# Kernel optimization log

Hardware: AMD Instinct MI355X
Metric: run time of the kernel (lower is better)

The kernel has to match this reference:

```python
import jax, jax.numpy as jnp
import numpy as np

N = 50000      # nodes
E = 800000     # edges (before self loops)
IN = 128       # input_dim
H1, C1 = 4, 64   # conv1 heads, per-head channels (concat -> 256)
H2, C2 = 1, 64   # conv2 heads, per-head channels (concat=False -> 64)
EPS_BN = 1e-5
NEG_SLOPE = 0.2


def setup_inputs() -> dict:
    key = jax.random.key(0)
    ks = jax.random.split(key, 20)
    s = 0.05
    d = {}
    d["x"] = jax.random.normal(ks[0], (N, IN), dtype=jnp.float32)
    d["edge_index"] = jax.random.randint(ks[1], (2, E), 0, N, dtype=jnp.int32)
    # GATConv 1: lin weight [IN, H1*C1], att vectors [H1, C1], bias [H1*C1]
    d["W1"] = jax.random.normal(ks[2], (IN, H1 * C1), dtype=jnp.float32) * s
    d["a1_src"] = jax.random.normal(ks[3], (H1, C1), dtype=jnp.float32) * s
    d["a1_dst"] = jax.random.normal(ks[4], (H1, C1), dtype=jnp.float32) * s
    d["b1"] = jnp.zeros((H1 * C1,), jnp.float32)
    # GATConv 2 (concat=False): lin weight [H1*C1, H2*C2]
    d["W2"] = jax.random.normal(ks[5], (H1 * C1, H2 * C2), dtype=jnp.float32) * s
    d["a2_src"] = jax.random.normal(ks[6], (H2, C2), dtype=jnp.float32) * s
    d["a2_dst"] = jax.random.normal(ks[7], (H2, C2), dtype=jnp.float32) * s
    d["b2"] = jnp.zeros((C2,), jnp.float32)
    # projection Linear(output_dim -> input_dim)
    d["Wp"] = jax.random.normal(ks[8], (C2, IN), dtype=jnp.float32) * s
    d["bp"] = jnp.zeros((IN,), jnp.float32)
    # BatchNorm affine params
    d["g1"] = jnp.ones((H1 * C1,), jnp.float32); d["be1"] = jnp.zeros((H1 * C1,), jnp.float32)
    d["g2"] = jnp.ones((C2,), jnp.float32);      d["be2"] = jnp.zeros((C2,), jnp.float32)
    d["g3"] = jnp.ones((IN,), jnp.float32);      d["be3"] = jnp.zeros((IN,), jnp.float32)
    return d


def batch_norm(x, gamma, beta):
    mu = jnp.mean(x, axis=0, keepdims=True)
    var = jnp.var(x, axis=0, keepdims=True)
    return (x - mu) * jax.lax.rsqrt(var + EPS_BN) * gamma + beta


def gat_conv(x, src, dst, W, a_src, a_dst, bias, heads, out_ch, concat):
    n = x.shape[0]
    h = (x @ W).reshape(n, heads, out_ch)            # [N,H,C]
    alpha_s = jnp.einsum('nhc,hc->nh', h, a_src)     # [N,H]
    alpha_d = jnp.einsum('nhc,hc->nh', h, a_dst)
    e = jax.nn.leaky_relu(alpha_s[src] + alpha_d[dst], NEG_SLOPE)  # [E',H]
    # segment softmax over edges sharing the same destination node
    m = jax.ops.segment_max(e, dst, num_segments=n)
    m = jnp.where(jnp.isfinite(m), m, 0.0)
    ex = jnp.exp(e - m[dst])
    den = jax.ops.segment_sum(ex, dst, num_segments=n)
    alpha = ex / (den[dst] + 1e-16)                  # [E',H]
    msg = alpha[:, :, None] * h[src]                 # [E',H,C]
    out = jax.ops.segment_sum(msg, dst, num_segments=n)  # [N,H,C]
    if concat:
        out = out.reshape(n, heads * out_ch)
    else:
        out = out.mean(axis=1)
    return out + bias


def reference(x, edge_index, W1, a1_src, a1_dst, b1, W2, a2_src, a2_dst, b2,
              Wp, bp, g1, be1, g2, be2, g3, be3):
    n = x.shape[0]
    # PyG GATConv default add_self_loops=True
    loops = jnp.arange(n, dtype=edge_index.dtype)
    src = jnp.concatenate([edge_index[0], loops])
    dst = jnp.concatenate([edge_index[1], loops])
    h = gat_conv(x, src, dst, W1, a1_src, a1_dst, b1, H1, C1, True)
    h = jax.nn.elu(batch_norm(h, g1, be1))
    # dropout is a no-op in eval mode
    h = gat_conv(h, src, dst, W2, a2_src, a2_dst, b2, H2, C2, False)
    h = jax.nn.elu(batch_norm(h, g2, be2))
    h = h @ Wp + bp
    return batch_norm(h, g3, be3)
```

## Files before the change

kernel.cpp:

```cpp
#include <hip/hip_runtime.h>
#include <cstdint>
#include <cstddef>

#define NEG_SLOPE 0.2f
#define EPS_BN 1e-5f

typedef __bf16 bf16x8 __attribute__((ext_vector_type(8)));
typedef float  f32x4  __attribute__((ext_vector_type(4)));
typedef unsigned short ushort_t;

static __device__ __forceinline__ float lrelu(float x){ return x > 0.f ? x : NEG_SLOPE * x; }

static __device__ __forceinline__ float bf2f(ushort_t u){
  union { unsigned i; float f; } c; c.i = ((unsigned)u) << 16; return c.f;
}
static __device__ __forceinline__ ushort_t f2bf(float f){
  unsigned u = __float_as_uint(f);
  u += 0x7fffu + ((u >> 16) & 1u);
  return (ushort_t)(u >> 16);
}
static __device__ __forceinline__ void unpk(unsigned u, float& lo, float& hi){
  lo = __uint_as_float(u << 16);
  hi = __uint_as_float(u & 0xffff0000u);
}

static inline int ceil_div(int a, int b){ return (a + b - 1) / b; }


__global__ void fill_u32_kernel(unsigned* __restrict__ p, unsigned v, int n){
  int i = blockIdx.x * 256 + threadIdx.x;
  if(i < n) p[i] = v;
}

__global__ void f2bf_kernel(const float* __restrict__ in, ushort_t* __restrict__ out, long n){
  long i = ((long)blockIdx.x * 256 + threadIdx.x) * 4;
  if(i + 3 < n){
    float4 v = *reinterpret_cast<const float4*>(in + i);
    ushort_t t0 = f2bf(v.x), t1 = f2bf(v.y), t2 = f2bf(v.z), t3 = f2bf(v.w);
    uint2 pk; pk.x = t0 | ((unsigned)t1 << 16); pk.y = t2 | ((unsigned)t3 << 16);
    *reinterpret_cast<uint2*>(out + i) = pk;
  } else {
    for(; i < n; i++) out[i] = f2bf(in[i]);
  }
}


__global__ void hist_kernel(const int* __restrict__ ei, int* __restrict__ deg, int E, int N){
  int e = blockIdx.x * 256 + threadIdx.x;
  if(e >= E + N) return;
  int d = (e < E) ? ei[E + e] : (e - E);
  atomicAdd(&deg[d], 1);
}

__global__ __launch_bounds__(256) void scan1_kernel(const int* __restrict__ deg, int* __restrict__ rowptr,
                                                    int* __restrict__ cur, int* __restrict__ partials, int n){
  int t = threadIdx.x, lane = t & 63, wv = t >> 6;
  int base = blockIdx.x * 2048 + t * 8;
  int v[8]; int run = 0;
  #pragma unroll
  for(int k = 0; k < 8; k++){ int i = base + k; v[k] = (i < n) ? deg[i] : 0; run += v[k]; }
  int sc = run;
  #pragma unroll
  for(int off = 1; off < 64; off <<= 1){
    int u = __shfl_up(sc, off);
    if(lane >= off) sc += u;
  }
  __shared__ int wtot[4], woff[4];
  if(lane == 63) wtot[wv] = sc;
  __syncthreads();
  if(t == 0){
    int a = 0;
    #pragma unroll
    for(int i = 0; i < 4; i++){ woff[i] = a; a += wtot[i]; }
    partials[blockIdx.x] = a;
  }
  __syncthreads();
  int excl = (sc - run) + woff[wv];
  #pragma unroll
  for(int k = 0; k < 8; k++){
    int i = base + k;
    if(i < n){ cur[i] = excl; excl += v[k]; rowptr[i + 1] = excl; }
  }
}

__global__ void scan2_kernel(int* __restrict__ partials, int nb){
  int lane = threadIdx.x;
  int v = (lane < nb) ? partials[lane] : 0;
  int sc = v;
  #pragma unroll
  for(int off = 1; off < 64; off <<= 1){
    int u = __shfl_up(sc, off);
    if(lane >= off) sc += u;
  }
  if(lane < nb) partials[lane] = sc - v;
}

__global__ void scan3_kernel(const int* __restrict__ partials, int* __restrict__ rowptr,
                             int* __restrict__ cur, int n){
  int i = blockIdx.x * 256 + threadIdx.x;
  if(i == 0) rowptr[0] = 0;
  if(i < n){
    int off = partials[i >> 11];
    rowptr[i + 1] += off;
    cur[i] += off;
  }
}

__global__ void scatter_kernel(const int* __restrict__ ei, int* __restrict__ cur,
                               int* __restrict__ col, int* __restrict__ row, int E, int N){
  int e = blockIdx.x * 256 + threadIdx.x;
  if(e >= E + N) return;
  int s, d;
  if(e < E){ s = ei[e]; d = ei[E + e]; } else { s = e - E; d = e - E; }
  int pos = atomicAdd(&cur[d], 1);
  col[pos] = s;
  row[pos] = d;
}


__global__ void packW_kernel(const float* __restrict__ W, ushort_t* __restrict__ Wp, int K, int Nn){
  int idx = blockIdx.x * 256 + threadIdx.x;
  int KS = K >> 5;
  int total = (Nn >> 4) * KS * 64;
  if(idx >= total) return;
  int lane = idx & 63;
  int rest = idx >> 6;
  int s = rest % KS, t = rest / KS;
  int n  = t * 16 + (lane & 15);
  int k0 = s * 32 + (lane >> 4) * 8;
  ushort_t tmp[8];
  #pragma unroll
  for(int j = 0; j < 8; j++) tmp[j] = f2bf(W[(size_t)(k0 + j) * Nn + n]);
  uint4 pk;
  pk.x = tmp[0] | ((unsigned)tmp[1] << 16);
  pk.y = tmp[2] | ((unsigned)tmp[3] << 16);
  pk.z = tmp[4] | ((unsigned)tmp[5] << 16);
  pk.w = tmp[6] | ((unsigned)tmp[7] << 16);
  *reinterpret_cast<uint4*>(Wp + (size_t)idx * 8) = pk;
}


template<int K, bool OUT_BF16, bool DO_ALPHA>
__global__ __launch_bounds__(256) void gemm_mfma_kernel(const ushort_t* __restrict__ A,
                                                        const ushort_t* __restrict__ Bp,
                                                        void* __restrict__ C, int M, int Nn,
                                                        const float* __restrict__ a_src,
                                                        const float* __restrict__ a_dst,
                                                        float* __restrict__ as_,
                                                        float* __restrict__ ad_){
  constexpr int KS = K >> 5;
  int lane = threadIdx.x & 63, wv = threadIdx.x >> 6;
  int row0 = blockIdx.x * 64 + wv * 16;
  int col0 = blockIdx.y * 64;
  int mi = lane & 15, q = lane >> 4;
  const bf16x8* arow = reinterpret_cast<const bf16x8*>(A + (size_t)(row0 + mi) * K + q * 8);
  const bf16x8* bbase = reinterpret_cast<const bf16x8*>(Bp) + ((size_t)(col0 >> 4) * KS) * 64 + lane;
  f32x4 acc[4] = {};
  #pragma unroll
  for(int s = 0; s < KS; s++){
    bf16x8 af = arow[s * 4];
    #pragma unroll
    for(int t = 0; t < 4; t++){
      bf16x8 bfr = bbase[((size_t)t * KS + s) * 64];
      acc[t] = __builtin_amdgcn_mfma_f32_16x16x32_bf16(af, bfr, acc[t], 0, 0, 0);
    }
  }
  #pragma unroll
  for(int t = 0; t < 4; t++){
    #pragma unroll
    for(int r = 0; r < 4; r++){
      int gr = row0 + q * 4 + r;
      if(gr < M){
        int gc = col0 + t * 16 + mi;
        float v = acc[t][r];
        if(OUT_BF16) ((ushort_t*)C)[(size_t)gr * Nn + gc] = f2bf(v);
        else         ((float*)   C)[(size_t)gr * Nn + gc] = v;
      }
    }
  }
  if(DO_ALPHA){
    const int H = Nn >> 6;
    int head = blockIdx.y;
    #pragma unroll
    for(int r = 0; r < 4; r++){
      int gr = row0 + q * 4 + r;
      float ps = 0.f, pd = 0.f;
      #pragma unroll
      for(int t = 0; t < 4; t++){
        float av = acc[t][r];
        int c = head * 64 + t * 16 + mi;
        ps += av * a_src[c];
        pd += av * a_dst[c];
      }
      #pragma unroll
      for(int off = 1; off < 16; off <<= 1){
        ps += __shfl_xor(ps, off);
        pd += __shfl_xor(pd, off);
      }
      if(mi == 0 && gr < M){
        as_[(size_t)gr * H + head] = ps;
        ad_[(size_t)gr * H + head] = pd;
      }
    }
  }
}


template<int H>
__global__ void edgew_kernel(const int* __restrict__ col, const int* __restrict__ row,
                             const float* __restrict__ as_, const float* __restrict__ ad_,
                             float* __restrict__ w, int EP){
  int j = blockIdx.x * 256 + threadIdx.x;
  if(j >= EP) return;
  int s = col[j], d = row[j];
  #pragma unroll
  for(int h = 0; h < H; h++){
    float e = lrelu(as_[s * H + h] + ad_[d * H + h]);
    w[(size_t)j * H + h] = __expf(e);
  }
}


__global__ __launch_bounds__(256) void gat_aggregate4_kernel(const ushort_t* __restrict__ hfeat,
                                                             const float* __restrict__ w,
                                                             const int* __restrict__ rowptr,
                                                             const int* __restrict__ col,
                                                             const float* __restrict__ bias,
                                                             float* __restrict__ out, int N){
  int wid = threadIdx.x >> 6, lane = threadIdx.x & 63;
  int n = blockIdx.x * 4 + wid;
  if(n >= N) return;
  int start = rowptr[n], end = rowptr[n + 1];
  int g = lane >> 5, l = lane & 31;
  int hidx = l >> 3;
  float d0 = 0.f, d1 = 0.f, d2 = 0.f, d3 = 0.f;
  for(int j = start + lane; j < end; j += 64){
    float4 wv4 = *reinterpret_cast<const float4*>(w + (size_t)j * 4);
    d0 += wv4.x; d1 += wv4.y; d2 += wv4.z; d3 += wv4.w;
  }
  #pragma unroll
  for(int off = 32; off; off >>= 1){
    d0 += __shfl_xor(d0, off); d1 += __shfl_xor(d1, off);
    d2 += __shfl_xor(d2, off); d3 += __shfl_xor(d3, off);
  }
  float den = (hidx == 0) ? d0 : (hidx == 1) ? d1 : (hidx == 2) ? d2 : d3;
  float dinv = 1.f / (den + 1e-16f);
  float acc[8] = {};
  auto body = [&](int j){
    int s = col[j];
    float wj = w[(size_t)j * 4 + hidx];
    uint4 u = *reinterpret_cast<const uint4*>(hfeat + (size_t)s * 256 + 8 * l);
    float a, b;
    unpk(u.x, a, b); acc[0] += wj * a; acc[1] += wj * b;
    unpk(u.y, a, b); acc[2] += wj * a; acc[3] += wj * b;
    unpk(u.z, a, b); acc[4] += wj * a; acc[5] += wj * b;
    unpk(u.w, a, b); acc[6] += wj * a; acc[7] += wj * b;
  };
  int j = start + g;
  for(; j + 2 < end; j += 4){ body(j); body(j + 2); }
  if(j < end) body(j);
  #pragma unroll
  for(int k = 0; k < 8; k++) acc[k] += __shfl_xor(acc[k], 32);
  int cbase = 8 * l + g * 4;
  float4 o;
  o.x = acc[g * 4 + 0] * dinv + bias[cbase + 0];
  o.y = acc[g * 4 + 1] * dinv + bias[cbase + 1];
  o.z = acc[g * 4 + 2] * dinv + bias[cbase + 2];
  o.w = acc[g * 4 + 3] * dinv + bias[cbase + 3];
  *reinterpret_cast<float4*>(out + (size_t)n * 256 + cbase) = o;
}


__global__ __launch_bounds__(256) void gat_aggregate1_kernel(const ushort_t* __restrict__ hfeat,
                                                             const float* __restrict__ w,
                                                             const int* __restrict__ rowptr,
                                                             const int* __restrict__ col,
                                                             const float* __restrict__ bias,
                                                             float* __restrict__ out, int N){
  int wid = threadIdx.x >> 6, lane = threadIdx.x & 63;
  int n = blockIdx.x * 4 + wid;
  if(n >= N) return;
  int start = rowptr[n], end = rowptr[n + 1];
  int g = lane >> 4, l = lane & 15;
  float den = 0.f;
  for(int j = start + lane; j < end; j += 64) den += w[j];
  #pragma unroll
  for(int off = 32; off; off >>= 1) den += __shfl_xor(den, off);
  float dinv = 1.f / (den + 1e-16f);
  float acc[4] = {};
  auto body = [&](int j){
    int s = col[j];
    float wj = w[j];
    uint2 u = *reinterpret_cast<const uint2*>(hfeat + (size_t)s * 64 + 4 * l);
    float a, b;
    unpk(u.x, a, b); acc[0] += wj * a; acc[1] += wj * b;
    unpk(u.y, a, b); acc[2] += wj * a; acc[3] += wj * b;
  };
  int j = start + g;
  for(; j + 4 < end; j += 8){ body(j); body(j + 4); }
  if(j < end) body(j);
  #pragma unroll
  for(int k = 0; k < 4; k++){
    acc[k] += __shfl_xor(acc[k], 16);
    acc[k] += __shfl_xor(acc[k], 32);
  }
  if(g == 0){
    float4 o;
    o.x = acc[0] * dinv + bias[4 * l + 0];
    o.y = acc[1] * dinv + bias[4 * l + 1];
    o.z = acc[2] * dinv + bias[4 * l + 2];
    o.w = acc[3] * dinv + bias[4 * l + 3];
    *reinterpret_cast<float4*>(out + (size_t)n * 64 + 4 * l) = o;
  }
}


__global__ __launch_bounds__(256) void colstats_kernel(const float* __restrict__ x, float* __restrict__ stats, int N, int C){
  int t = threadIdx.x;
  int rpb = 256 / C;
  int c = t % C;
  int rg = t / C;
  float sum = 0.f, sq = 0.f;
  for(int r = blockIdx.x * rpb + rg; r < N; r += gridDim.x * rpb){
    float v = x[(size_t)r * C + c];
    sum += v; sq += v * v;
  }
  __shared__ float ssum[256], ssq[256];
  ssum[t] = sum; ssq[t] = sq;
  __syncthreads();
  if(t < C){
    float S = 0.f, Q = 0.f;
    for(int g = 0; g < rpb; g++){ S += ssum[g * C + t]; Q += ssq[g * C + t]; }
    atomicAdd(&stats[t], S);
    atomicAdd(&stats[C + t], Q);
  }
}

template<bool OUT_BF16>
__global__ void bn_act_kernel(const float* __restrict__ x, const float* __restrict__ stats,
                              const float* __restrict__ gamma, const float* __restrict__ beta,
                              void* __restrict__ y, int N, int C, int do_elu){
  size_t i = (size_t)blockIdx.x * 256 + threadIdx.x;
  if(i >= (size_t)N * C) return;
  int c = (int)(i & (size_t)(C - 1));
  float invN = 1.f / (float)N;
  float mu = stats[c] * invN;
  float var = stats[C + c] * invN - mu * mu;
  float v = (x[i] - mu) * rsqrtf(var + EPS_BN) * gamma[c] + beta[c];
  if(do_elu) v = v > 0.f ? v : expm1f(v);
  if(OUT_BF16) ((ushort_t*)y)[i] = f2bf(v);
  else         ((float*)y)[i]    = v;
}


extern "C" void kernel_launch(void* const* d_in, const int* in_sizes, int n_in,
                              void* d_out, int out_size, void* d_ws, size_t ws_size,
                              hipStream_t stream){
  const float* x   = (const float*)d_in[0];
  const int*   ei  = (const int*)  d_in[1];
  const float* W1  = (const float*)d_in[2];
  const float* a1s = (const float*)d_in[3];
  const float* a1d = (const float*)d_in[4];
  const float* b1  = (const float*)d_in[5];
  const float* W2  = (const float*)d_in[6];
  const float* a2s = (const float*)d_in[7];
  const float* a2d = (const float*)d_in[8];
  const float* b2  = (const float*)d_in[9];
  const float* Wp  = (const float*)d_in[10];
  const float* g1  = (const float*)d_in[12]; const float* be1 = (const float*)d_in[13];
  const float* g2  = (const float*)d_in[14]; const float* be2 = (const float*)d_in[15];
  const float* g3  = (const float*)d_in[16]; const float* be3 = (const float*)d_in[17];
  float* out = (float*)d_out;

  const int N  = in_sizes[0] / 128;
  const int E  = in_sizes[1] / 2;
  const int EP = E + N;
  const int Mpad = ((N + 63) / 64) * 64;
  const int NB = ceil_div(N, 2048);

  char* p = (char*)d_ws;
  auto carve = [&](size_t bytes) -> char* {
    char* r = p; p += (bytes + 255) & ~(size_t)255; return r;
  };
  int*   deg    = (int*)carve((size_t)N * 4);
  int*   cur    = (int*)carve((size_t)N * 4);
  int*   rowptr = (int*)carve((size_t)(N + 1) * 4);
  int*   col    = (int*)carve((size_t)EP * 4);
  int*   row    = (int*)carve((size_t)EP * 4);
  int*   part   = (int*)carve(64 * 4);
  float* as_    = (float*)carve((size_t)N * 4 * 4);
  float* ad_    = (float*)carve((size_t)N * 4 * 4);
  float* stats  = (float*)carve(512 * 4);
  ushort_t* W1p = (ushort_t*)carve((size_t)128 * 256 * 2);
  ushort_t* W2p = (ushort_t*)carve((size_t)256 * 64 * 2);
  ushort_t* W3p = (ushort_t*)carve((size_t)64 * 128 * 2);
  char* S1 = carve((size_t)Mpad * 256 * 2);
  ushort_t* h1b   = (ushort_t*)S1;
  ushort_t* act1b = (ushort_t*)S1;
  float*    h3    = (float*)S1;
  char* S2 = carve((size_t)N * 256 * 4);
  ushort_t* xb    = (ushort_t*)S2;
  float*    out1  = (float*)S2;
  ushort_t* h2b   = (ushort_t*)S2;
  float*    out2  = (float*)(S2 + (((size_t)Mpad * 64 * 2 + 255) & ~(size_t)255));
  ushort_t* act2b = (ushort_t*)((char*)out2 + (((size_t)N * 64 * 4 + 255) & ~(size_t)255));
  float* w_edge = (float*)carve((size_t)EP * 4 * 4);

  fill_u32_kernel<<<ceil_div(N, 256), 256, 0, stream>>>((unsigned*)deg, 0u, N);
  hist_kernel<<<ceil_div(EP, 256), 256, 0, stream>>>(ei, deg, E, N);
  scan1_kernel<<<NB, 256, 0, stream>>>(deg, rowptr, cur, part, N);
  scan2_kernel<<<1, 64, 0, stream>>>(part, NB);
  scan3_kernel<<<ceil_div(N, 256), 256, 0, stream>>>(part, rowptr, cur, N);
  scatter_kernel<<<ceil_div(EP, 256), 256, 0, stream>>>(ei, cur, col, row, E, N);

  f2bf_kernel<<<ceil_div(N * 128 / 4, 256), 256, 0, stream>>>(x, xb, (long)N * 128);
  packW_kernel<<<ceil_div(16 * 4 * 64, 256), 256, 0, stream>>>(W1, W1p, 128, 256);
  packW_kernel<<<ceil_div(4 * 8 * 64, 256), 256, 0, stream>>>(W2, W2p, 256, 64);
  packW_kernel<<<ceil_div(8 * 2 * 64, 256), 256, 0, stream>>>(Wp, W3p, 64, 128);

  gemm_mfma_kernel<128, true, true><<<dim3(Mpad / 64, 4), 256, 0, stream>>>(xb, W1p, h1b, N, 256, a1s, a1d, as_, ad_);
  edgew_kernel<4><<<ceil_div(EP, 256), 256, 0, stream>>>(col, row, as_, ad_, w_edge, EP);
  gat_aggregate4_kernel<<<ceil_div(N, 4), 256, 0, stream>>>(h1b, w_edge, rowptr, col, b1, out1, N);
  fill_u32_kernel<<<2, 256, 0, stream>>>((unsigned*)stats, 0u, 512);
  colstats_kernel<<<512, 256, 0, stream>>>(out1, stats, N, 256);
  bn_act_kernel<true><<<ceil_div(N * 256, 256), 256, 0, stream>>>(out1, stats, g1, be1, act1b, N, 256, 1);

  gemm_mfma_kernel<256, true, true><<<dim3(Mpad / 64, 1), 256, 0, stream>>>(act1b, W2p, h2b, N, 64, a2s, a2d, as_, ad_);
  edgew_kernel<1><<<ceil_div(EP, 256), 256, 0, stream>>>(col, row, as_, ad_, w_edge, EP);
  gat_aggregate1_kernel<<<ceil_div(N, 4), 256, 0, stream>>>(h2b, w_edge, rowptr, col, b2, out2, N);
  fill_u32_kernel<<<2, 256, 0, stream>>>((unsigned*)stats, 0u, 512);
  colstats_kernel<<<512, 256, 0, stream>>>(out2, stats, N, 64);
  bn_act_kernel<true><<<ceil_div(N * 64, 256), 256, 0, stream>>>(out2, stats, g2, be2, act2b, N, 64, 1);

  gemm_mfma_kernel<64, false, false><<<dim3(Mpad / 64, 2), 256, 0, stream>>>(act2b, W3p, h3, N, 128, nullptr, nullptr, nullptr, nullptr);
  fill_u32_kernel<<<2, 256, 0, stream>>>((unsigned*)stats, 0u, 512);
  colstats_kernel<<<512, 256, 0, stream>>>(h3, stats, N, 128);
  bn_act_kernel<false><<<ceil_div(N * 128, 256), 256, 0, stream>>>(h3, stats, g3, be3, out, N, 128, 0);
}
```

Before: 487.1 us.

## Fuse edge weights, BN+ELU and bf16 conversion into GEMM and aggregation kernels

Edge-weight kernels are removed, and the aggregation kernels now compute the exp(leaky_relu) attention weights inline, caching up to CAP of them per node in shared memory. BatchNorm becomes a colstats kernel that computes scale and shift in its last block via an atomic ticket, and the following GEMM applies scale, shift and ELU while loading A. Intermediate tensors are stored in bf16, the x-to-bf16 conversion moves into the first GEMM, and the three weight packs run as one launch. Together this cuts launches and intermediate memory traffic, at the cost of bf16 rounding of the pre-BN tensors and exp recomputation for nodes with degree above CAP.

```diff
diff --git a/kernel.cpp b/kernel.cpp
--- a/kernel.cpp
+++ b/kernel.cpp
@@ -4,12 +4,14 @@
 
 #define NEG_SLOPE 0.2f
 #define EPS_BN 1e-5f
+#define CAP 128
 
 typedef __bf16 bf16x8 __attribute__((ext_vector_type(8)));
 typedef float  f32x4  __attribute__((ext_vector_type(4)));
 typedef unsigned short ushort_t;
 
 static __device__ __forceinline__ float lrelu(float x){ return x > 0.f ? x : NEG_SLOPE * x; }
+static __device__ __forceinline__ float elu(float x){ return x > 0.f ? x : __expf(x) - 1.f; }
 
 static __device__ __forceinline__ float bf2f(ushort_t u){
   union { unsigned i; float f; } c; c.i = ((unsigned)u) << 16; return c.f;
@@ -24,24 +26,14 @@
   hi = __uint_as_float(u & 0xffff0000u);
 }
 
+union BF8 { bf16x8 v; ushort_t u[8]; };
+
 static inline int ceil_div(int a, int b){ return (a + b - 1) / b; }
 
 
 __global__ void fill_u32_kernel(unsigned* __restrict__ p, unsigned v, int n){
   int i = blockIdx.x * 256 + threadIdx.x;
   if(i < n) p[i] = v;
-}
-
-__global__ void f2bf_kernel(const float* __restrict__ in, ushort_t* __restrict__ out, long n){
-  long i = ((long)blockIdx.x * 256 + threadIdx.x) * 4;
-  if(i + 3 < n){
-    float4 v = *reinterpret_cast<const float4*>(in + i);
-    ushort_t t0 = f2bf(v.x), t1 = f2bf(v.y), t2 = f2bf(v.z), t3 = f2bf(v.w);
-    uint2 pk; pk.x = t0 | ((unsigned)t1 << 16); pk.y = t2 | ((unsigned)t3 << 16);
-    *reinterpret_cast<uint2*>(out + i) = pk;
-  } else {
-    for(; i < n; i++) out[i] = f2bf(in[i]);
-  }
 }
 
 
@@ -107,24 +99,20 @@
 }
 
 __global__ void scatter_kernel(const int* __restrict__ ei, int* __restrict__ cur,
-                               int* __restrict__ col, int* __restrict__ row, int E, int N){
+                               int* __restrict__ col, int E, int N){
   int e = blockIdx.x * 256 + threadIdx.x;
   if(e >= E + N) return;
   int s, d;
   if(e < E){ s = ei[e]; d = ei[E + e]; } else { s = e - E; d = e - E; }
   int pos = atomicAdd(&cur[d], 1);
   col[pos] = s;
-  row[pos] = d;
-}
-
-
-__global__ void packW_kernel(const float* __restrict__ W, ushort_t* __restrict__ Wp, int K, int Nn){
-  int idx = blockIdx.x * 256 + threadIdx.x;
-  int KS = K >> 5;
-  int total = (Nn >> 4) * KS * 64;
-  if(idx >= total) return;
+}
+
+
+static __device__ void packW_body(const float* W, ushort_t* Wp, int K, int Nn, int idx){
   int lane = idx & 63;
   int rest = idx >> 6;
+  int KS = K >> 5;
   int s = rest % KS, t = rest / KS;
   int n  = t * 16 + (lane & 15);
   int k0 = s * 32 + (lane >> 4) * 8;
@@ -139,116 +127,142 @@
   *reinterpret_cast<uint4*>(Wp + (size_t)idx * 8) = pk;
 }
 
-
-template<int K, bool OUT_BF16, bool DO_ALPHA>
-__global__ __launch_bounds__(256) void gemm_mfma_kernel(const ushort_t* __restrict__ A,
-                                                        const ushort_t* __restrict__ Bp,
-                                                        void* __restrict__ C, int M, int Nn,
-                                                        const float* __restrict__ a_src,
-                                                        const float* __restrict__ a_dst,
-                                                        float* __restrict__ as_,
-                                                        float* __restrict__ ad_){
+__global__ void packW_all_kernel(const float* __restrict__ W1, const float* __restrict__ W2,
+                                 const float* __restrict__ W3, ushort_t* __restrict__ W1p,
+                                 ushort_t* __restrict__ W2p, ushort_t* __restrict__ W3p){
+  int idx = blockIdx.x * 256 + threadIdx.x;
+  if(idx < 4096)       packW_body(W1, W1p, 128, 256, idx);
+  else if(idx < 6144)  packW_body(W2, W2p, 256, 64,  idx - 4096);
+  else if(idx < 7168)  packW_body(W3, W3p, 64,  128, idx - 6144);
+}
+
+
+template<int K, int NT, int AMODE, int H>
+__global__ __launch_bounds__(256) void gemm_kernel(const void* __restrict__ Asrc,
+                                                   const ushort_t* __restrict__ Bp,
+                                                   ushort_t* __restrict__ C, int M,
+                                                   const float* __restrict__ scale,
+                                                   const float* __restrict__ shift,
+                                                   const float* __restrict__ a_src,
+                                                   const float* __restrict__ a_dst,
+                                                   float* __restrict__ as_,
+                                                   float* __restrict__ ad_){
   constexpr int KS = K >> 5;
   int lane = threadIdx.x & 63, wv = threadIdx.x >> 6;
   int row0 = blockIdx.x * 64 + wv * 16;
-  int col0 = blockIdx.y * 64;
   int mi = lane & 15, q = lane >> 4;
-  const bf16x8* arow = reinterpret_cast<const bf16x8*>(A + (size_t)(row0 + mi) * K + q * 8);
-  const bf16x8* bbase = reinterpret_cast<const bf16x8*>(Bp) + ((size_t)(col0 >> 4) * KS) * 64 + lane;
-  f32x4 acc[4] = {};
+  int arow = row0 + mi; if(arow > M - 1) arow = M - 1;
+  const bf16x8* bbase = reinterpret_cast<const bf16x8*>(Bp) + lane;
+  f32x4 acc[NT] = {};
   #pragma unroll
   for(int s = 0; s < KS; s++){
-    bf16x8 af = arow[s * 4];
+    BF8 cv;
+    if(AMODE == 0){
+      const float* ap = (const float*)Asrc + (size_t)arow * K + s * 32 + q * 8;
+      float4 u0 = *reinterpret_cast<const float4*>(ap);
+      float4 u1 = *reinterpret_cast<const float4*>(ap + 4);
+      cv.u[0] = f2bf(u0.x); cv.u[1] = f2bf(u0.y); cv.u[2] = f2bf(u0.z); cv.u[3] = f2bf(u0.w);
+      cv.u[4] = f2bf(u1.x); cv.u[5] = f2bf(u1.y); cv.u[6] = f2bf(u1.z); cv.u[7] = f2bf(u1.w);
+    } else {
+      const ushort_t* ap = (const ushort_t*)Asrc + (size_t)arow * K + s * 32 + q * 8;
+      uint4 u = *reinterpret_cast<const uint4*>(ap);
+      int c0 = s * 32 + q * 8;
+      float4 sc0 = *reinterpret_cast<const float4*>(scale + c0);
+      float4 sc1 = *reinterpret_cast<const float4*>(scale + c0 + 4);
+      float4 sh0 = *reinterpret_cast<const float4*>(shift + c0);
+      float4 sh1 = *reinterpret_cast<const float4*>(shift + c0 + 4);
+      float a, b;
+      unpk(u.x, a, b); cv.u[0] = f2bf(elu(a * sc0.x + sh0.x)); cv.u[1] = f2bf(elu(b * sc0.y + sh0.y));
+      unpk(u.y, a, b); cv.u[2] = f2bf(elu(a * sc0.z + sh0.z)); cv.u[3] = f2bf(elu(b * sc0.w + sh0.w));
+      unpk(u.z, a, b); cv.u[4] = f2bf(elu(a * sc1.x + sh1.x)); cv.u[5] = f2bf(elu(b * sc1.y + sh1.y));
+      unpk(u.w, a, b); cv.u[6] = f2bf(elu(a * sc1.z + sh1.z)); cv.u[7] = f2bf(elu(b * sc1.w + sh1.w));
+    }
+    bf16x8 af = cv.v;
     #pragma unroll
-    for(int t = 0; t < 4; t++){
+    for(int t = 0; t < NT; t++){
       bf16x8 bfr = bbase[((size_t)t * KS + s) * 64];
       acc[t] = __builtin_amdgcn_mfma_f32_16x16x32_bf16(af, bfr, acc[t], 0, 0, 0);
     }
   }
   #pragma unroll
-  for(int t = 0; t < 4; t++){
+  for(int t = 0; t < NT; t++){
     #pragma unroll
     for(int r = 0; r < 4; r++){
       int gr = row0 + q * 4 + r;
-      if(gr < M){
-        int gc = col0 + t * 16 + mi;
-        float v = acc[t][r];
-        if(OUT_BF16) ((ushort_t*)C)[(size_t)gr * Nn + gc] = f2bf(v);
-        else         ((float*)   C)[(size_t)gr * Nn + gc] = v;
+      if(gr < M) C[(size_t)gr * (NT * 16) + t * 16 + mi] = f2bf(acc[t][r]);
+    }
+  }
+  if(H > 0){
+    #pragma unroll
+    for(int hh = 0; hh < H; hh++){
+      #pragma unroll
+      for(int r = 0; r < 4; r++){
+        float ps = 0.f, pd = 0.f;
+        #pragma unroll
+        for(int tt = 0; tt < 4; tt++){
+          int t = hh * 4 + tt;
+          float av = acc[t][r];
+          int c = t * 16 + mi;
+          ps += av * a_src[c];
+          pd += av * a_dst[c];
+        }
+        #pragma unroll
+        for(int off = 1; off < 16; off <<= 1){
+          ps += __shfl_xor(ps, off);
+          pd += __shfl_xor(pd, off);
+        }
+        int gr = row0 + q * 4 + r;
+        if(mi == 0 && gr < M){
+          as_[(size_t)gr * H + hh] = ps;
+          ad_[(size_t)gr * H + hh] = pd;
+        }
       }
     }
   }
-  if(DO_ALPHA){
-    const int H = Nn >> 6;
-    int head = blockIdx.y;
-    #pragma unroll
-    for(int r = 0; r < 4; r++){
-      int gr = row0 + q * 4 + r;
-      float ps = 0.f, pd = 0.f;
-      #pragma unroll
-      for(int t = 0; t < 4; t++){
-        float av = acc[t][r];
-        int c = head * 64 + t * 16 + mi;
-        ps += av * a_src[c];
-        pd += av * a_dst[c];
-      }
-      #pragma unroll
-      for(int off = 1; off < 16; off <<= 1){
-        ps += __shfl_xor(ps, off);
-        pd += __shfl_xor(pd, off);
-      }
-      if(mi == 0 && gr < M){
-        as_[(size_t)gr * H + head] = ps;
-        ad_[(size_t)gr * H + head] = pd;
-      }
-    }
-  }
-}
-
-
-template<int H>
-__global__ void edgew_kernel(const int* __restrict__ col, const int* __restrict__ row,
-                             const float* __restrict__ as_, const float* __restrict__ ad_,
-                             float* __restrict__ w, int EP){
-  int j = blockIdx.x * 256 + threadIdx.x;
-  if(j >= EP) return;
-  int s = col[j], d = row[j];
-  #pragma unroll
-  for(int h = 0; h < H; h++){
-    float e = lrelu(as_[s * H + h] + ad_[d * H + h]);
-    w[(size_t)j * H + h] = __expf(e);
-  }
-}
-
-
-__global__ __launch_bounds__(256) void gat_aggregate4_kernel(const ushort_t* __restrict__ hfeat,
-                                                             const float* __restrict__ w,
-                                                             const int* __restrict__ rowptr,
-                                                             const int* __restrict__ col,
-                                                             const float* __restrict__ bias,
-                                                             float* __restrict__ out, int N){
+}
+
+
+__global__ __launch_bounds__(256) void gat_agg4_kernel(const ushort_t* __restrict__ hfeat,
+                                                       const float* __restrict__ as_,
+                                                       const float* __restrict__ ad_,
+                                                       const int* __restrict__ rowptr,
+                                                       const int* __restrict__ col,
+                                                       const float* __restrict__ bias,
+                                                       ushort_t* __restrict__ out, int N){
+  __shared__ float wsh[4][CAP * 4];
   int wid = threadIdx.x >> 6, lane = threadIdx.x & 63;
   int n = blockIdx.x * 4 + wid;
-  if(n >= N) return;
+  if(n > N - 1) n = N - 1;
   int start = rowptr[n], end = rowptr[n + 1];
-  int g = lane >> 5, l = lane & 31;
-  int hidx = l >> 3;
+  float4 adn = *reinterpret_cast<const float4*>(ad_ + (size_t)n * 4);
   float d0 = 0.f, d1 = 0.f, d2 = 0.f, d3 = 0.f;
   for(int j = start + lane; j < end; j += 64){
-    float4 wv4 = *reinterpret_cast<const float4*>(w + (size_t)j * 4);
-    d0 += wv4.x; d1 += wv4.y; d2 += wv4.z; d3 += wv4.w;
+    int s = col[j];
+    float4 av = *reinterpret_cast<const float4*>(as_ + (size_t)s * 4);
+    float w0 = __expf(lrelu(av.x + adn.x));
+    float w1 = __expf(lrelu(av.y + adn.y));
+    float w2 = __expf(lrelu(av.z + adn.z));
+    float w3 = __expf(lrelu(av.w + adn.w));
+    int jj = j - start;
+    if(jj < CAP) *reinterpret_cast<float4*>(&wsh[wid][jj * 4]) = make_float4(w0, w1, w2, w3);
+    d0 += w0; d1 += w1; d2 += w2; d3 += w3;
   }
   #pragma unroll
   for(int off = 32; off; off >>= 1){
     d0 += __shfl_xor(d0, off); d1 += __shfl_xor(d1, off);
     d2 += __shfl_xor(d2, off); d3 += __shfl_xor(d3, off);
   }
+  __syncthreads();
+  int g = lane >> 5, l = lane & 31, hidx = l >> 3;
   float den = (hidx == 0) ? d0 : (hidx == 1) ? d1 : (hidx == 2) ? d2 : d3;
   float dinv = 1.f / (den + 1e-16f);
+  float adh = (hidx == 0) ? adn.x : (hidx == 1) ? adn.y : (hidx == 2) ? adn.z : adn.w;
   float acc[8] = {};
   auto body = [&](int j){
     int s = col[j];
-    float wj = w[(size_t)j * 4 + hidx];
+    int jj = j - start;
+    float wj = (jj < CAP) ? wsh[wid][jj * 4 + hidx]
+                          : __expf(lrelu(as_[(size_t)s * 4 + hidx] + adh));
     uint4 u = *reinterpret_cast<const uint4*>(hfeat + (size_t)s * 256 + 8 * l);
     float a, b;
     unpk(u.x, a, b); acc[0] += wj * a; acc[1] += wj * b;
@@ -262,35 +276,46 @@
   #pragma unroll
   for(int k = 0; k < 8; k++) acc[k] += __shfl_xor(acc[k], 32);
   int cbase = 8 * l + g * 4;
-  float4 o;
-  o.x = acc[g * 4 + 0] * dinv + bias[cbase + 0];
-  o.y = acc[g * 4 + 1] * dinv + bias[cbase + 1];
-  o.z = acc[g * 4 + 2] * dinv + bias[cbase + 2];
-  o.w = acc[g * 4 + 3] * dinv + bias[cbase + 3];
-  *reinterpret_cast<float4*>(out + (size_t)n * 256 + cbase) = o;
-}
-
-
-__global__ __launch_bounds__(256) void gat_aggregate1_kernel(const ushort_t* __restrict__ hfeat,
-                                                             const float* __restrict__ w,
-                                                             const int* __restrict__ rowptr,
-                                                             const int* __restrict__ col,
-                                                             const float* __restrict__ bias,
-                                                             float* __restrict__ out, int N){
+  ushort_t o0 = f2bf(acc[g * 4 + 0] * dinv + bias[cbase + 0]);
+  ushort_t o1 = f2bf(acc[g * 4 + 1] * dinv + bias[cbase + 1]);
+  ushort_t o2 = f2bf(acc[g * 4 + 2] * dinv + bias[cbase + 2]);
+  ushort_t o3 = f2bf(acc[g * 4 + 3] * dinv + bias[cbase + 3]);
+  uint2 pk; pk.x = o0 | ((unsigned)o1 << 16); pk.y = o2 | ((unsigned)o3 << 16);
+  *reinterpret_cast<uint2*>(out + (size_t)n * 256 + cbase) = pk;
+}
+
+
+__global__ __launch_bounds__(256) void gat_agg1_kernel(const ushort_t* __restrict__ hfeat,
+                                                       const float* __restrict__ as_,
+                                                       const float* __restrict__ ad_,
+                                                       const int* __restrict__ rowptr,
+                                                       const int* __restrict__ col,
+                                                       const float* __restrict__ bias,
+                                                       ushort_t* __restrict__ out, int N){
+  __shared__ float wsh[4][CAP];
   int wid = threadIdx.x >> 6, lane = threadIdx.x & 63;
   int n = blockIdx.x * 4 + wid;
-  if(n >= N) return;
+  if(n > N - 1) n = N - 1;
   int start = rowptr[n], end = rowptr[n + 1];
+  float adn = ad_[n];
+  float den = 0.f;
+  for(int j = start + lane; j < end; j += 64){
+    int s = col[j];
+    float w = __expf(lrelu(as_[s] + adn));
+    int jj = j - start;
+    if(jj < CAP) wsh[wid][jj] = w;
+    den += w;
+  }
+  #pragma unroll
+  for(int off = 32; off; off >>= 1) den += __shfl_xor(den, off);
+  __syncthreads();
+  float dinv = 1.f / (den + 1e-16f);
   int g = lane >> 4, l = lane & 15;
-  float den = 0.f;
-  for(int j = start + lane; j < end; j += 64) den += w[j];
-  #pragma unroll
-  for(int off = 32; off; off >>= 1) den += __shfl_xor(den, off);
-  float dinv = 1.f / (den + 1e-16f);
   float acc[4] = {};
   auto body = [&](int j){
     int s = col[j];
-    float wj = w[j];
+    int jj = j - start;
+    float wj = (jj < CAP) ? wsh[wid][jj] : __expf(lrelu(as_[s] + adn));
     uint2 u = *reinterpret_cast<const uint2*>(hfeat + (size_t)s * 64 + 4 * l);
     float a, b;
     unpk(u.x, a, b); acc[0] += wj * a; acc[1] += wj * b;
@@ -305,24 +330,29 @@
     acc[k] += __shfl_xor(acc[k], 32);
   }
   if(g == 0){
-    float4 o;
-    o.x = acc[0] * dinv + bias[4 * l + 0];
-    o.y = acc[1] * dinv + bias[4 * l + 1];
-    o.z = acc[2] * dinv + bias[4 * l + 2];
-    o.w = acc[3] * dinv + bias[4 * l + 3];
-    *reinterpret_cast<float4*>(out + (size_t)n * 64 + 4 * l) = o;
-  }
-}
-
-
-__global__ __launch_bounds__(256) void colstats_kernel(const float* __restrict__ x, float* __restrict__ stats, int N, int C){
+    ushort_t o0 = f2bf(acc[0] * dinv + bias[4 * l + 0]);
+    ushort_t o1 = f2bf(acc[1] * dinv + bias[4 * l + 1]);
+    ushort_t o2 = f2bf(acc[2] * dinv + bias[4 * l + 2]);
+    ushort_t o3 = f2bf(acc[3] * dinv + bias[4 * l + 3]);
+    uint2 pk; pk.x = o0 | ((unsigned)o1 << 16); pk.y = o2 | ((unsigned)o3 << 16);
+    *reinterpret_cast<uint2*>(out + (size_t)n * 64 + 4 * l) = pk;
+  }
+}
+
+
+__global__ __launch_bounds__(256) void colstats_fin_kernel(const ushort_t* __restrict__ x, int N, int C,
+                                                           float* __restrict__ stats,
+                                                           const float* __restrict__ gamma,
+                                                           const float* __restrict__ beta,
+                                                           float* __restrict__ scale,
+                                                           float* __restrict__ shift,
+                                                           unsigned* __restrict__ ticket, int nblk){
   int t = threadIdx.x;
   int rpb = 256 / C;
-  int c = t % C;
-  int rg = t / C;
+  int c = t % C, rg = t / C;
   float sum = 0.f, sq = 0.f;
   for(int r = blockIdx.x * rpb + rg; r < N; r += gridDim.x * rpb){
-    float v = x[(size_t)r * C + c];
+    float v = bf2f(x[(size_t)r * C + c]);
     sum += v; sq += v * v;
   }
   __shared__ float ssum[256], ssq[256];
@@ -334,22 +364,36 @@
     atomicAdd(&stats[t], S);
     atomicAdd(&stats[C + t], Q);
   }
-}
-
-template<bool OUT_BF16>
-__global__ void bn_act_kernel(const float* __restrict__ x, const float* __restrict__ stats,
-                              const float* __restrict__ gamma, const float* __restrict__ beta,
-                              void* __restrict__ y, int N, int C, int do_elu){
-  size_t i = (size_t)blockIdx.x * 256 + threadIdx.x;
-  if(i >= (size_t)N * C) return;
-  int c = (int)(i & (size_t)(C - 1));
-  float invN = 1.f / (float)N;
-  float mu = stats[c] * invN;
-  float var = stats[C + c] * invN - mu * mu;
-  float v = (x[i] - mu) * rsqrtf(var + EPS_BN) * gamma[c] + beta[c];
-  if(do_elu) v = v > 0.f ? v : expm1f(v);
-  if(OUT_BF16) ((ushort_t*)y)[i] = f2bf(v);
-  else         ((float*)y)[i]    = v;
+  __shared__ bool is_last;
+  __syncthreads();
+  if(t == 0){
+    __threadfence();
+    unsigned prev = atomicAdd(ticket, 1u);
+    is_last = (prev == (unsigned)(nblk - 1));
+  }
+  __syncthreads();
+  if(is_last){
+    for(int cc = t; cc < C; cc += 256){
+      float S = atomicAdd(&stats[cc], 0.f);
+      float Q = atomicAdd(&stats[C + cc], 0.f);
+      float invN = 1.f / (float)N;
+      float mu = S * invN;
+      float var = Q * invN - mu * mu;
+      float rs = rsqrtf(var + EPS_BN);
+      float scl = rs * gamma[cc];
+      scale[cc] = scl;
+      shift[cc] = beta[cc] - mu * scl;
+    }
+  }
+}
+
+
+__global__ void bn3_kernel(const ushort_t* __restrict__ x, const float* __restrict__ scale,
+                           const float* __restrict__ shift, float* __restrict__ y, long total, int cmask){
+  long i = (long)blockIdx.x * 256 + threadIdx.x;
+  if(i >= total) return;
+  int c = (int)(i & (long)cmask);
+  y[i] = bf2f(x[i]) * scale[c] + shift[c];
 }
 
 
@@ -382,58 +426,45 @@
   auto carve = [&](size_t bytes) -> char* {
     char* r = p; p += (bytes + 255) & ~(size_t)255; return r;
   };
+  float* meta   = (float*)carve(2048 * 4);
   int*   deg    = (int*)carve((size_t)N * 4);
   int*   cur    = (int*)carve((size_t)N * 4);
   int*   rowptr = (int*)carve((size_t)(N + 1) * 4);
   int*   col    = (int*)carve((size_t)EP * 4);
-  int*   row    = (int*)carve((size_t)EP * 4);
   int*   part   = (int*)carve(64 * 4);
   float* as_    = (float*)carve((size_t)N * 4 * 4);
   float* ad_    = (float*)carve((size_t)N * 4 * 4);
-  float* stats  = (float*)carve(512 * 4);
   ushort_t* W1p = (ushort_t*)carve((size_t)128 * 256 * 2);
   ushort_t* W2p = (ushort_t*)carve((size_t)256 * 64 * 2);
   ushort_t* W3p = (ushort_t*)carve((size_t)64 * 128 * 2);
-  char* S1 = carve((size_t)Mpad * 256 * 2);
-  ushort_t* h1b   = (ushort_t*)S1;
-  ushort_t* act1b = (ushort_t*)S1;
-  float*    h3    = (float*)S1;
-  char* S2 = carve((size_t)N * 256 * 4);
-  ushort_t* xb    = (ushort_t*)S2;
-  float*    out1  = (float*)S2;
-  ushort_t* h2b   = (ushort_t*)S2;
-  float*    out2  = (float*)(S2 + (((size_t)Mpad * 64 * 2 + 255) & ~(size_t)255));
-  ushort_t* act2b = (ushort_t*)((char*)out2 + (((size_t)N * 64 * 4 + 255) & ~(size_t)255));
-  float* w_edge = (float*)carve((size_t)EP * 4 * 4);
-
-  fill_u32_kernel<<<ceil_div(N, 256), 256, 0, stream>>>((unsigned*)deg, 0u, N);
+  ushort_t* h1b   = (ushort_t*)carve((size_t)Mpad * 256 * 2);
+  ushort_t* out1b = (ushort_t*)carve((size_t)Mpad * 256 * 2);
+  ushort_t* h2b   = (ushort_t*)carve((size_t)Mpad * 64 * 2);
+  ushort_t* out2b = (ushort_t*)carve((size_t)Mpad * 64 * 2);
+  ushort_t* h3b   = (ushort_t*)carve((size_t)Mpad * 128 * 2);
+
+  float* stats1 = meta;        float* scale1 = meta + 512;  float* shift1 = meta + 768;
+  float* stats2 = meta + 1024; float* scale2 = meta + 1152; float* shift2 = meta + 1216;
+  float* stats3 = meta + 1280; float* scale3 = meta + 1536; float* shift3 = meta + 1664;
+  unsigned* tick = (unsigned*)(meta + 1792);
+
+  fill_u32_kernel<<<ceil_div(N + 2048, 256), 256, 0, stream>>>((unsigned*)meta, 0u, N + 2048);
   hist_kernel<<<ceil_div(EP, 256), 256, 0, stream>>>(ei, deg, E, N);
   scan1_kernel<<<NB, 256, 0, stream>>>(deg, rowptr, cur, part, N);
   scan2_kernel<<<1, 64, 0, stream>>>(part, NB);
   scan3_kernel<<<ceil_div(N, 256), 256, 0, stream>>>(part, rowptr, cur, N);
-  scatter_kernel<<<ceil_div(EP, 256), 256, 0, stream>>>(ei, cur, col, row, E, N);
-
-  f2bf_kernel<<<ceil_div(N * 128 / 4, 256), 256, 0, stream>>>(x, xb, (long)N * 128);
-  packW_kernel<<<ceil_div(16 * 4 * 64, 256), 256, 0, stream>>>(W1, W1p, 128, 256);
-  packW_kernel<<<ceil_div(4 * 8 * 64, 256), 256, 0, stream>>>(W2, W2p, 256, 64);
-  packW_kernel<<<ceil_div(8 * 2 * 64, 256), 256, 0, stream>>>(Wp, W3p, 64, 128);
-
-  gemm_mfma_kernel<128, true, true><<<dim3(Mpad / 64, 4), 256, 0, stream>>>(xb, W1p, h1b, N, 256, a1s, a1d, as_, ad_);
-  edgew_kernel<4><<<ceil_div(EP, 256), 256, 0, stream>>>(col, row, as_, ad_, w_edge, EP);
-  gat_aggregate4_kernel<<<ceil_div(N, 4), 256, 0, stream>>>(h1b, w_edge, rowptr, col, b1, out1, N);
-  fill_u32_kernel<<<2, 256, 0, stream>>>((unsigned*)stats, 0u, 512);
-  colstats_kernel<<<512, 256, 0, stream>>>(out1, stats, N, 256);
-  bn_act_kernel<true><<<ceil_div(N * 256, 256), 256, 0, stream>>>(out1, stats, g1, be1, act1b, N, 256, 1);
-
-  gemm_mfma_kernel<256, true, true><<<dim3(Mpad / 64, 1), 256, 0, stream>>>(act1b, W2p, h2b, N, 64, a2s, a2d, as_, ad_);
-  edgew_kernel<1><<<ceil_div(EP, 256), 256, 0, stream>>>(col, row, as_, ad_, w_edge, EP);
-  gat_aggregate1_kernel<<<ceil_div(N, 4), 256, 0, stream>>>(h2b, w_edge, rowptr, col, b2, out2, N);
-  fill_u32_kernel<<<2, 256, 0, stream>>>((unsigned*)stats, 0u, 512);
-  colstats_kernel<<<512, 256, 0, stream>>>(out2, stats, N, 64);
-  bn_act_kernel<true><<<ceil_div(N * 64, 256), 256, 0, stream>>>(out2, stats, g2, be2, act2b, N, 64, 1);
-
-  gemm_mfma_kernel<64, false, false><<<dim3(Mpad / 64, 2), 256, 0, stream>>>(act2b, W3p, h3, N, 128, nullptr, nullptr, nullptr, nullptr);
-  fill_u32_kernel<<<2, 256, 0, stream>>>((unsigned*)stats, 0u, 512);
-  colstats_kernel<<<512, 256, 0, stream>>>(h3, stats, N, 128);
-  bn_act_kernel<false><<<ceil_div(N * 128, 256), 256, 0, stream>>>(h3, stats, g3, be3, out, N, 128, 0);
-}
+  scatter_kernel<<<ceil_div(EP, 256), 256, 0, stream>>>(ei, cur, col, E, N);
+  packW_all_kernel<<<28, 256, 0, stream>>>(W1, W2, Wp, W1p, W2p, W3p);
+
+  gemm_kernel<128, 16, 0, 4><<<Mpad / 64, 256, 0, stream>>>(x, W1p, h1b, N, nullptr, nullptr, a1s, a1d, as_, ad_);
+  gat_agg4_kernel<<<ceil_div(N, 4), 256, 0, stream>>>(h1b, as_, ad_, rowptr, col, b1, out1b, N);
+  colstats_fin_kernel<<<512, 256, 0, stream>>>(out1b, N, 256, stats1, g1, be1, scale1, shift1, tick + 0, 512);
+
+  gemm_kernel<256, 4, 1, 1><<<Mpad / 64, 256, 0, stream>>>(out1b, W2p, h2b, N, scale1, shift1, a2s, a2d, as_, ad_);
+  gat_agg1_kernel<<<ceil_div(N, 4), 256, 0, stream>>>(h2b, as_, ad_, rowptr, col, b2, out2b, N);
+  colstats_fin_kernel<<<512, 256, 0, stream>>>(out2b, N, 64, stats2, g2, be2, scale2, shift2, tick + 1, 512);
+
+  gemm_kernel<64, 8, 1, 0><<<Mpad / 64, 256, 0, stream>>>(out2b, W3p, h3b, N, scale2, shift2, nullptr, nullptr, nullptr, nullptr);
+  colstats_fin_kernel<<<512, 256, 0, stream>>>(h3b, N, 128, stats3, g3, be3, scale3, shift3, tick + 2, 512);
+  bn3_kernel<<<ceil_div(N * 128, 256), 256, 0, stream>>>(h3b, scale3, shift3, out, (long)N * 128, 127);
+}
```

Result: no change. 480.5 us (-1.4%).
